# Kernel tuning notes

Hardware: AMD Instinct MI355X
Metric: run time of the kernel (lower is better)

Reference implementation:

```python
import jax, jax.numpy as jnp
import numpy as np

EPSILON = 0.1
SOFT_WEIGHT = 0.1
SOFT_LAMBDA = 0.2


def setup_inputs() -> dict:
    key = jax.random.key(0)
    k1, k2, k3 = jax.random.split(key, 3)
    B, C, P = 4096, 32000, 50
    inputs = jax.random.normal(k1, (B, C), dtype=jnp.float32)
    targets = jax.random.randint(k2, (B,), 0, C, dtype=jnp.int64)
    all_posvid = jax.random.randint(k3, (B, P), 0, C, dtype=jnp.int64)
    return {"inputs": inputs, "targets": targets, "all_posvid": all_posvid}


def reference(inputs, targets, all_posvid):
    B, C = inputs.shape
    P = all_posvid.shape[1]
    log_probs = jax.nn.log_softmax(inputs, axis=1)  # [B, C]

    # Per-row unique+counts then scatter is equivalent to a batched histogram:
    # soft_targets[i, c] = soft_lambda * count(c in all_posvid[i]) / P
    row_idx = jnp.broadcast_to(jnp.arange(B)[:, None], all_posvid.shape)
    soft_targets = jnp.zeros((B, C), dtype=log_probs.dtype).at[row_idx, all_posvid].add(
        SOFT_LAMBDA / P
    )

    onehot = jax.nn.one_hot(targets, C, dtype=log_probs.dtype)  # [B, C]

    # soft_label=True branch
    soft_targets = (1.0 - SOFT_LAMBDA) * onehot + soft_targets
    smoothed = (1.0 - EPSILON) * onehot + EPSILON / C

    loss_hard = (-smoothed * log_probs).mean(0).sum()
    loss_soft = (-soft_targets * log_probs).mean(0).sum()
    return loss_hard * (1.0 - SOFT_WEIGHT) + loss_soft * SOFT_WEIGHT
```

## Files before the change

### kernel.cpp

```cpp
#include <hip/hip_runtime.h>
#include <math.h>


#define NB 4096
#define NC 32000
#define NP 50
#define NF4 (NC / 4)

typedef float f4 __attribute__((ext_vector_type(4)));

__global__ __launch_bounds__(256) void row_loss_kernel(
    const float* __restrict__ x,
    const int*   __restrict__ targets,
    const int*   __restrict__ posvid,
    float*       __restrict__ row_loss)
{
    const int row = blockIdx.x;
    const int tid = threadIdx.x;
    const float* __restrict__ xr = x + (size_t)row * NC;
    const f4*    __restrict__ x4 = (const f4*)xr;

    float e0 = 0.0f, e1 = 0.0f, e2 = 0.0f, e3 = 0.0f;
    float t0 = 0.0f, t1 = 0.0f, t2 = 0.0f, t3 = 0.0f;

    int idx = tid;
    for (; idx + 3 * 256 < NF4; idx += 4 * 256) {
        f4 a = x4[idx];
        f4 b = x4[idx + 256];
        f4 c = x4[idx + 512];
        f4 d = x4[idx + 768];

        e0 += __expf(a.x); e1 += __expf(a.y); e2 += __expf(a.z); e3 += __expf(a.w);
        t0 += a.x;         t1 += a.y;         t2 += a.z;         t3 += a.w;

        e0 += __expf(b.x); e1 += __expf(b.y); e2 += __expf(b.z); e3 += __expf(b.w);
        t0 += b.x;         t1 += b.y;         t2 += b.z;         t3 += b.w;

        e0 += __expf(c.x); e1 += __expf(c.y); e2 += __expf(c.z); e3 += __expf(c.w);
        t0 += c.x;         t1 += c.y;         t2 += c.z;         t3 += c.w;

        e0 += __expf(d.x); e1 += __expf(d.y); e2 += __expf(d.z); e3 += __expf(d.w);
        t0 += d.x;         t1 += d.y;         t2 += d.z;         t3 += d.w;
    }
    for (; idx < NF4; idx += 256) {
        f4 a = x4[idx];
        e0 += __expf(a.x); e1 += __expf(a.y); e2 += __expf(a.z); e3 += __expf(a.w);
        t0 += a.x;         t1 += a.y;         t2 += a.z;         t3 += a.w;
    }

    float s    = (e0 + e1) + (e2 + e3);
    float sumx = (t0 + t1) + (t2 + t3);

    __shared__ float ss[256];
    __shared__ float sx[256];
    ss[tid] = s; sx[tid] = sumx;
    __syncthreads();

    for (int off = 128; off > 0; off >>= 1) {
        if (tid < off) {
            ss[tid] += ss[tid + off];
            sx[tid] += sx[tid + off];
        }
        __syncthreads();
    }

    float g = 0.0f;
    if (tid < NP) {
        int c = posvid[(size_t)row * NP + tid];
        g = xr[c];
    }
    if (tid < 64) {
#pragma unroll
        for (int off = 32; off > 0; off >>= 1)
            g += __shfl_down(g, off, 64);
    }

    if (tid == 0) {
        const float EPSILON     = 0.1f;
        const float SOFT_WEIGHT = 0.1f;
        const float SOFT_LAMBDA = 0.2f;
        const float A  = (1.0f - SOFT_WEIGHT) * (1.0f - EPSILON)
                       + SOFT_WEIGHT * (1.0f - SOFT_LAMBDA);
        const float C1 = (1.0f - SOFT_WEIGHT) * EPSILON / (float)NC;
        const float C2 = SOFT_WEIGHT * SOFT_LAMBDA / (float)NP;

        float lse  = logf(ss[0]);
        float loss = -( A  * (xr[targets[row]] - lse)
                      + C1 * (sx[0] - (float)NC * lse)
                      + C2 * (g     - (float)NP * lse) );
        row_loss[row] = loss;
    }
}

__global__ __launch_bounds__(256) void reduce_kernel(
    const float* __restrict__ rl, float* __restrict__ out)
{
    __shared__ float sm[256];
    const int tid = threadIdx.x;
    float acc = 0.0f;
    for (int i = tid; i < NB; i += 256)
        acc += rl[i];
    sm[tid] = acc;
    __syncthreads();
    for (int off = 128; off > 0; off >>= 1) {
        if (tid < off) sm[tid] += sm[tid + off];
        __syncthreads();
    }
    if (tid == 0) out[0] = sm[0] * (1.0f / (float)NB);
}

extern "C" void kernel_launch(void* const* d_in, const int* in_sizes, int n_in,
                              void* d_out, int out_size, void* d_ws, size_t ws_size,
                              hipStream_t stream)
{
    const float* x       = (const float*)d_in[0];
    const int*   targets = (const int*)d_in[1];
    const int*   posvid  = (const int*)d_in[2];
    float*       out     = (float*)d_out;
    float*       ws      = (float*)d_ws;

    row_loss_kernel<<<NB, 256, 0, stream>>>(x, targets, posvid, ws);
    reduce_kernel<<<1, 256, 0, stream>>>(ws, out);
}
```

Baseline: 99.84 us.

## Split each row across two blocks and combine partial sums in final kernel

Each row's 32000 logits are now handled by two blocks, one per half, giving 8192 blocks. Each block writes partial exp-sum and x-sum into an 8-float per-row workspace, and the final single-block kernel does the log-sum-exp and loss per row. The shared-memory tree reductions are replaced with wavefront shuffles and a small cross-wave step. This aims for more parallelism and less per-block reduction overhead on a bandwidth-bound pass, at the cost of more serial work in the single combine block.

Measured after the change: 95.91 us, median of 2. 3.9% less time.

```diff
diff --git a/kernel.cpp b/kernel.cpp
--- a/kernel.cpp
+++ b/kernel.cpp
@@ -5,26 +5,27 @@
 #define NB 4096
 #define NC 32000
 #define NP 50
-#define NF4 (NC / 4)
+#define NF4H 4000
 
 typedef float f4 __attribute__((ext_vector_type(4)));
 
-__global__ __launch_bounds__(256) void row_loss_kernel(
+__global__ __launch_bounds__(256) void row_half_kernel(
     const float* __restrict__ x,
     const int*   __restrict__ targets,
     const int*   __restrict__ posvid,
-    float*       __restrict__ row_loss)
+    float*       __restrict__ rw)
 {
-    const int row = blockIdx.x;
-    const int tid = threadIdx.x;
+    const int row  = blockIdx.x >> 1;
+    const int half = blockIdx.x & 1;
+    const int tid  = threadIdx.x;
     const float* __restrict__ xr = x + (size_t)row * NC;
-    const f4*    __restrict__ x4 = (const f4*)xr;
+    const f4*    __restrict__ x4 = (const f4*)xr + half * NF4H;
 
     float e0 = 0.0f, e1 = 0.0f, e2 = 0.0f, e3 = 0.0f;
     float t0 = 0.0f, t1 = 0.0f, t2 = 0.0f, t3 = 0.0f;
 
     int idx = tid;
-    for (; idx + 3 * 256 < NF4; idx += 4 * 256) {
+    for (; idx + 3 * 256 < NF4H; idx += 4 * 256) {
         f4 a = x4[idx];
         f4 b = x4[idx + 256];
         f4 c = x4[idx + 512];
@@ -32,17 +33,14 @@
 
         e0 += __expf(a.x); e1 += __expf(a.y); e2 += __expf(a.z); e3 += __expf(a.w);
         t0 += a.x;         t1 += a.y;         t2 += a.z;         t3 += a.w;
-
         e0 += __expf(b.x); e1 += __expf(b.y); e2 += __expf(b.z); e3 += __expf(b.w);
         t0 += b.x;         t1 += b.y;         t2 += b.z;         t3 += b.w;
-
         e0 += __expf(c.x); e1 += __expf(c.y); e2 += __expf(c.z); e3 += __expf(c.w);
         t0 += c.x;         t1 += c.y;         t2 += c.z;         t3 += c.w;
-
         e0 += __expf(d.x); e1 += __expf(d.y); e2 += __expf(d.z); e3 += __expf(d.w);
         t0 += d.x;         t1 += d.y;         t2 += d.z;         t3 += d.w;
     }
-    for (; idx < NF4; idx += 256) {
+    for (; idx < NF4H; idx += 256) {
         f4 a = x4[idx];
         e0 += __expf(a.x); e1 += __expf(a.y); e2 += __expf(a.z); e3 += __expf(a.w);
         t0 += a.x;         t1 += a.y;         t2 += a.z;         t3 += a.w;
@@ -51,62 +49,84 @@
     float s    = (e0 + e1) + (e2 + e3);
     float sumx = (t0 + t1) + (t2 + t3);
 
-    __shared__ float ss[256];
-    __shared__ float sx[256];
-    ss[tid] = s; sx[tid] = sumx;
-    __syncthreads();
-
-    for (int off = 128; off > 0; off >>= 1) {
-        if (tid < off) {
-            ss[tid] += ss[tid + off];
-            sx[tid] += sx[tid + off];
-        }
-        __syncthreads();
+    const int lane = tid & 63;
+    const int wid  = tid >> 6;
+#pragma unroll
+    for (int off = 32; off > 0; off >>= 1) {
+        s    += __shfl_down(s, off, 64);
+        sumx += __shfl_down(sumx, off, 64);
     }
+    __shared__ float ls[4], lx[4];
+    if (lane == 0) { ls[wid] = s; lx[wid] = sumx; }
 
     float g = 0.0f;
-    if (tid < NP) {
+    if (half == 0 && tid < NP) {
         int c = posvid[(size_t)row * NP + tid];
         g = xr[c];
     }
-    if (tid < 64) {
+    __syncthreads();
+
+    if (half == 0 && tid < 64) {
 #pragma unroll
         for (int off = 32; off > 0; off >>= 1)
             g += __shfl_down(g, off, 64);
     }
 
     if (tid == 0) {
-        const float EPSILON     = 0.1f;
-        const float SOFT_WEIGHT = 0.1f;
-        const float SOFT_LAMBDA = 0.2f;
-        const float A  = (1.0f - SOFT_WEIGHT) * (1.0f - EPSILON)
-                       + SOFT_WEIGHT * (1.0f - SOFT_LAMBDA);
-        const float C1 = (1.0f - SOFT_WEIGHT) * EPSILON / (float)NC;
-        const float C2 = SOFT_WEIGHT * SOFT_LAMBDA / (float)NP;
-
-        float lse  = logf(ss[0]);
-        float loss = -( A  * (xr[targets[row]] - lse)
-                      + C1 * (sx[0] - (float)NC * lse)
-                      + C2 * (g     - (float)NP * lse) );
-        row_loss[row] = loss;
+        float S  = (ls[0] + ls[1]) + (ls[2] + ls[3]);
+        float SX = (lx[0] + lx[1]) + (lx[2] + lx[3]);
+        float* r8 = rw + (size_t)row * 8;
+        r8[half]     = S;
+        r8[2 + half] = SX;
+        if (half == 0) {
+            r8[4] = xr[targets[row]];
+            r8[5] = g;
+        }
     }
 }
 
-__global__ __launch_bounds__(256) void reduce_kernel(
-    const float* __restrict__ rl, float* __restrict__ out)
+__global__ __launch_bounds__(1024) void combine_kernel(
+    const float* __restrict__ rw, float* __restrict__ out)
 {
-    __shared__ float sm[256];
     const int tid = threadIdx.x;
+    const f4* __restrict__ w4 = (const f4*)rw;
+
+    const float EPSILON     = 0.1f;
+    const float SOFT_WEIGHT = 0.1f;
+    const float SOFT_LAMBDA = 0.2f;
+    const float A  = (1.0f - SOFT_WEIGHT) * (1.0f - EPSILON)
+                   + SOFT_WEIGHT * (1.0f - SOFT_LAMBDA);
+    const float C1 = (1.0f - SOFT_WEIGHT) * EPSILON / (float)NC;
+    const float C2 = SOFT_WEIGHT * SOFT_LAMBDA / (float)NP;
+
     float acc = 0.0f;
-    for (int i = tid; i < NB; i += 256)
-        acc += rl[i];
-    sm[tid] = acc;
+    for (int r = tid; r < NB; r += 1024) {
+        f4 a = w4[2 * r];
+        f4 b = w4[2 * r + 1];
+        float lse  = logf(a.x + a.y);
+        float sumx = a.z + a.w;
+        acc += -( A  * (b.x - lse)
+                + C1 * (sumx - (float)NC * lse)
+                + C2 * (b.y  - (float)NP * lse) );
+    }
+
+    const int lane = tid & 63;
+    const int wid  = tid >> 6;
+#pragma unroll
+    for (int off = 32; off > 0; off >>= 1)
+        acc += __shfl_down(acc, off, 64);
+
+    __shared__ float red[16];
+    if (lane == 0) red[wid] = acc;
     __syncthreads();
-    for (int off = 128; off > 0; off >>= 1) {
-        if (tid < off) sm[tid] += sm[tid + off];
-        __syncthreads();
+
+    if (tid < 16) {
+        float v = red[tid];
+#pragma unroll
+        for (int off = 8; off > 0; off >>= 1)
+            v += __shfl_down(v, off, 16);
+        if (tid == 0) out[0] = v * (1.0f / (float)NB);
     }
-    if (tid == 0) out[0] = sm[0] * (1.0f / (float)NB);
 }
 
 extern "C" void kernel_launch(void* const* d_in, const int* in_sizes, int n_in,
@@ -117,8 +137,8 @@
     const int*   targets = (const int*)d_in[1];
     const int*   posvid  = (const int*)d_in[2];
     float*       out     = (float*)d_out;
-    float*       ws      = (float*)d_ws;
+    float*       rw      = (float*)d_ws;
 
-    row_loss_kernel<<<NB, 256, 0, stream>>>(x, targets, posvid, ws);
-    reduce_kernel<<<1, 256, 0, stream>>>(ws, out);
+    row_half_kernel<<<2 * NB, 256, 0, stream>>>(x, targets, posvid, rw);
+    combine_kernel<<<1, 1024, 0, stream>>>(rw, out);
 }
```
